# Optimization experiments

Hardware: AMD Instinct MI355X
Metric: run time of the kernel (lower is better)

The kernel has to match this reference:

```python
import jax, jax.numpy as jnp
import numpy as np
import itertools

GRID = 256          # voxel grid extent per axis (coords in [0, GRID))
KSIZE = 3           # kernel_size
OFFSETS = np.array(list(itertools.product(range(KSIZE), repeat=3)), dtype=np.int32) - (KSIZE // 2)  # [27,3]


def setup_inputs() -> dict:
    key = jax.random.key(0)
    k1, k2, k3 = jax.random.split(key, 3)
    N, Cin, Cout = 262144, 64, 64
    coords = jax.random.randint(k1, (N, 3), 0, GRID, dtype=jnp.int32)
    feats = jax.random.normal(k2, (N, Cin), dtype=jnp.float32)
    kernel = jax.random.normal(k3, (KSIZE ** 3, Cin, Cout), dtype=jnp.float32) * 0.02
    return {"coords": coords, "feats": feats, "kernel": kernel}


def reference(coords, feats, kernel):
    # Submanifold sparse conv3d: out[i] = sum_k feats[j_k(i)] @ kernel[k]
    # where coords[j_k(i)] == coords[i] + offset_k (if such a point exists).
    N = coords.shape[0]
    Cout = kernel.shape[-1]
    # Hash table: linearized voxel -> point index (-1 if empty).
    lin = (coords[:, 0] * GRID + coords[:, 1]) * GRID + coords[:, 2]
    table = jnp.full((GRID ** 3,), -1, dtype=jnp.int32).at[lin].set(
        jnp.arange(N, dtype=jnp.int32))
    out = jnp.zeros((N, Cout), dtype=feats.dtype)
    for k in range(KSIZE ** 3):
        off = jnp.asarray(OFFSETS[k])              # [3]
        nc = coords + off[None, :]                 # neighbor coords [N,3]
        in_bounds = jnp.all((nc >= 0) & (nc < GRID), axis=1)
        nlin = (nc[:, 0] * GRID + nc[:, 1]) * GRID + nc[:, 2]
        idx = table[jnp.clip(nlin, 0, GRID ** 3 - 1)]
        valid = in_bounds & (idx >= 0)
        g = feats[jnp.where(valid, idx, 0)] * valid[:, None].astype(feats.dtype)  # [N,Cin]
        out = out + g @ kernel[k]                  # [N,Cout]
    return out
```

## Files before the change

### kernel.cpp

```cpp
#include <hip/hip_runtime.h>

#define VGRID 256
#define N_TAPS 27
#define CIN 64
#define COUT 64

typedef short short8 __attribute__((ext_vector_type(8)));
typedef float float4v __attribute__((ext_vector_type(4)));

__device__ __forceinline__ short f2bf(float x) {
    unsigned u = __builtin_bit_cast(unsigned, x);
    unsigned r = (u + 0x7FFF + ((u >> 16) & 1)) >> 16;
    return (short)r;
}

__global__ void __launch_bounds__(256) build_kernel(
        const int* __restrict__ coords, int* __restrict__ table,
        unsigned* __restrict__ bits, const float* __restrict__ W,
        short* __restrict__ Wt, int n, int bt_blocks) {
    if ((int)blockIdx.x >= bt_blocks) {
        int tap = blockIdx.x - bt_blocks;
        for (int e = threadIdx.x; e < CIN * COUT; e += 256) {
            int ci = e >> 6, co = e & 63;
            int ks = ci >> 5, quad = (ci >> 3) & 3, el = ci & 7;
            Wt[((((size_t)tap * 2 + ks) * 4 + quad) * 64 + co) * 8 + el] =
                f2bf(W[((size_t)tap * CIN + ci) * COUT + co]);
        }
        return;
    }
    int i = blockIdx.x * 256 + threadIdx.x;
    if (i >= n) return;
    int lin = (coords[i * 3 + 0] * VGRID + coords[i * 3 + 1]) * VGRID + coords[i * 3 + 2];
    atomicMax(&table[lin], i);
    atomicOr(&bits[lin >> 5], 1u << (lin & 31));
}

__global__ void __launch_bounds__(256) fused_kernel(
        const int* __restrict__ coords, const int* __restrict__ table,
        const unsigned* __restrict__ bits, const float* __restrict__ feats,
        const short* __restrict__ Wt, float* __restrict__ out, int n) {
    int t = threadIdx.x;
    int lane = t & 63;
    int i = blockIdx.x * 256 + t;
    int wbase = blockIdx.x * 256 + (t & 192);

    int cx = 0, cy = 0, cz = 0;
    unsigned hitmask = 0;
    int center_idx = 0;
    if (i < n) {
        cx = coords[i * 3 + 0];
        cy = coords[i * 3 + 1];
        cz = coords[i * 3 + 2];
        int clin = (cx * VGRID + cy) * VGRID + cz;
        center_idx = table[clin];

        int zlo = cz > 0 ? cz - 1 : 0;
        int zhi = cz < VGRID - 1 ? cz + 1 : VGRID - 1;
        int wlo = zlo >> 5, whi = zhi >> 5;
        unsigned rw0[9], rw1[9];
#pragma unroll
        for (int r = 0; r < 9; ++r) {
            int nx = cx + r / 3 - 1, ny = cy + r % 3 - 1;
            bool v = ((unsigned)nx < VGRID) && ((unsigned)ny < VGRID);
            int rb = ((nx * VGRID + ny) * VGRID) >> 5;
            rw0[r] = v ? bits[rb + wlo] : 0u;
            rw1[r] = v ? bits[rb + whi] : 0u;
        }
#pragma unroll
        for (int k = 0; k < N_TAPS; ++k) {
            if (k == 13) continue;
            int nz = cz + k % 3 - 1;
            if ((unsigned)nz < VGRID) {
                unsigned wrd = ((nz >> 5) == wlo) ? rw0[k / 3] : rw1[k / 3];
                hitmask |= ((wrd >> (nz & 31)) & 1u) << k;
            }
        }
    }

    int p0 = 0, p1 = 0, p2 = 0, p3 = 0;
    {
        unsigned hm = hitmask;
        int cnt = 0;
        while (hm) {
            int k = __builtin_ctz(hm); hm &= hm - 1u;
            int nlin = ((cx + k / 9 - 1) * VGRID + (cy + (k / 3) % 3 - 1)) * VGRID
                       + (cz + k % 3 - 1);
            int j = table[nlin];
            if (cnt == 0) p0 = j; else if (cnt == 1) p1 = j;
            else if (cnt == 2) p2 = j; else if (cnt == 3) p3 = j;
            ++cnt;
        }
    }

    int packed = (cx << 16) | (cy << 8) | cz;

    unsigned gmor = hitmask;
    gmor |= (unsigned)__shfl_xor((int)gmor, 1);
    gmor |= (unsigned)__shfl_xor((int)gmor, 2);
    gmor |= (unsigned)__shfl_xor((int)gmor, 4);
    gmor |= (unsigned)__shfl_xor((int)gmor, 8);

    int m = lane & 15, quad = lane >> 4;
    const short8* Bp = (const short8*)Wt;

    for (int g = 0; g < 4; ++g) {
        int src = g * 16 + m;
        int rpk = __shfl(packed, src);
        unsigned rhm = (unsigned)__shfl((int)hitmask, src);
        int rjc = __shfl(center_idx, src);
        int rp0 = __shfl(p0, src), rp1 = __shfl(p1, src);
        int rp2 = __shfl(p2, src), rp3 = __shfl(p3, src);
        unsigned gor = (unsigned)__shfl((int)gmor, g * 16);
        gor = __builtin_amdgcn_readfirstlane(gor);

        float4v acc[4] = {{0,0,0,0},{0,0,0,0},{0,0,0,0},{0,0,0,0}};

        {
            const float* fr = feats + (size_t)rjc * CIN + quad * 8;
            float4 u0 = *(const float4*)(fr);
            float4 u1 = *(const float4*)(fr + 4);
            float4 v0 = *(const float4*)(fr + 32);
            float4 v1 = *(const float4*)(fr + 36);
            short8 a0 = {f2bf(u0.x), f2bf(u0.y), f2bf(u0.z), f2bf(u0.w),
                         f2bf(u1.x), f2bf(u1.y), f2bf(u1.z), f2bf(u1.w)};
            short8 a1 = {f2bf(v0.x), f2bf(v0.y), f2bf(v0.z), f2bf(v0.w),
                         f2bf(v1.x), f2bf(v1.y), f2bf(v1.z), f2bf(v1.w)};
#pragma unroll
            for (int nt = 0; nt < 4; ++nt) {
                short8 b0 = Bp[((13 * 2 + 0) * 4 + quad) * 64 + nt * 16 + m];
                short8 b1 = Bp[((13 * 2 + 1) * 4 + quad) * 64 + nt * 16 + m];
                acc[nt] = __builtin_amdgcn_mfma_f32_16x16x32_bf16(a0, b0, acc[nt], 0, 0, 0);
                acc[nt] = __builtin_amdgcn_mfma_f32_16x16x32_bf16(a1, b1, acc[nt], 0, 0, 0);
            }
        }

        unsigned gm = gor;
        while (gm) {
            int k = (int)__builtin_ctz(gm); gm &= gm - 1u;
            bool has = (rhm >> k) & 1u;
            short8 h0 = {0,0,0,0,0,0,0,0}, h1 = {0,0,0,0,0,0,0,0};
            if (has) {
                int rank = __builtin_popcount(rhm & ((1u << k) - 1u));
                int j2;
                if (rank == 0) j2 = rp0;
                else if (rank == 1) j2 = rp1;
                else if (rank == 2) j2 = rp2;
                else if (rank == 3) j2 = rp3;
                else {
                    int rx = (rpk >> 16) & 255, ry = (rpk >> 8) & 255, rz = rpk & 255;
                    j2 = table[((rx + k / 9 - 1) * VGRID + (ry + (k / 3) % 3 - 1)) * VGRID
                               + (rz + k % 3 - 1)];
                }
                const float* hr = feats + (size_t)j2 * CIN + quad * 8;
                float4 u0 = *(const float4*)(hr);
                float4 u1 = *(const float4*)(hr + 4);
                float4 v0 = *(const float4*)(hr + 32);
                float4 v1 = *(const float4*)(hr + 36);
                h0 = (short8){f2bf(u0.x), f2bf(u0.y), f2bf(u0.z), f2bf(u0.w),
                              f2bf(u1.x), f2bf(u1.y), f2bf(u1.z), f2bf(u1.w)};
                h1 = (short8){f2bf(v0.x), f2bf(v0.y), f2bf(v0.z), f2bf(v0.w),
                              f2bf(v1.x), f2bf(v1.y), f2bf(v1.z), f2bf(v1.w)};
            }
#pragma unroll
            for (int nt = 0; nt < 4; ++nt) {
                short8 b0 = Bp[((k * 2 + 0) * 4 + quad) * 64 + nt * 16 + m];
                short8 b1 = Bp[((k * 2 + 1) * 4 + quad) * 64 + nt * 16 + m];
                acc[nt] = __builtin_amdgcn_mfma_f32_16x16x32_bf16(h0, b0, acc[nt], 0, 0, 0);
                acc[nt] = __builtin_amdgcn_mfma_f32_16x16x32_bf16(h1, b1, acc[nt], 0, 0, 0);
            }
        }

#pragma unroll
        for (int nt = 0; nt < 4; ++nt)
#pragma unroll
            for (int r2 = 0; r2 < 4; ++r2) {
                int orow = wbase + g * 16 + quad * 4 + r2;
                if (orow < n) out[(size_t)orow * COUT + nt * 16 + m] = acc[nt][r2];
            }
    }
}

extern "C" void kernel_launch(void* const* d_in, const int* in_sizes, int n_in,
                              void* d_out, int out_size, void* d_ws, size_t ws_size,
                              hipStream_t stream) {
    const int* coords = (const int*)d_in[0];
    const float* feats = (const float*)d_in[1];
    const float* weights = (const float*)d_in[2];
    float* out = (float*)d_out;

    int n = in_sizes[0] / 3;

    char* ws = (char*)d_ws;
    size_t BITMAP_BYTES = (size_t)VGRID * VGRID * VGRID / 8;
    unsigned* bits = (unsigned*)ws;
    short* wbft = (short*)(ws + BITMAP_BYTES);
    int* table = (int*)(ws + ((size_t)4 << 20));

    hipMemsetAsync(ws, 0, BITMAP_BYTES, stream);

    int bt_blocks = (n + 255) / 256;
    build_kernel<<<bt_blocks + N_TAPS, 256, 0, stream>>>(coords, table, bits,
                                                         weights, wbft, n, bt_blocks);

    fused_kernel<<<bt_blocks, 256, 0, stream>>>(coords, table, bits, feats,
                                                wbft, out, n);
}
```

Before: 222.6 us.

## Split neighbor lookup across two threads per point and stage metadata in LDS

Each block now handles 128 points with 256 threads. Two threads cooperate per point: each loads half of the bitmap rows and does up to two table lookups, and the results are combined through shared memory. Each wave then runs two 16-row MFMA groups instead of four, which doubles the grid size and increases parallelism for the latency-bound gather phase. The cost is two block barriers, extra LDS traffic, and a launch-bounds occupancy hint that may limit registers.

```diff
diff --git a/kernel.cpp b/kernel.cpp
--- a/kernel.cpp
+++ b/kernel.cpp
@@ -4,6 +4,7 @@
 #define N_TAPS 27
 #define CIN 64
 #define COUT 64
+#define BPTS 128
 
 typedef short short8 __attribute__((ext_vector_type(8)));
 typedef float float4v __attribute__((ext_vector_type(4)));
@@ -35,82 +36,102 @@
     atomicOr(&bits[lin >> 5], 1u << (lin & 31));
 }
 
-__global__ void __launch_bounds__(256) fused_kernel(
+__global__ void __launch_bounds__(256, 8) fused_kernel(
         const int* __restrict__ coords, const int* __restrict__ table,
         const unsigned* __restrict__ bits, const float* __restrict__ feats,
         const short* __restrict__ Wt, float* __restrict__ out, int n) {
+    __shared__ int s_pk[BPTS];
+    __shared__ unsigned s_hm[2][BPTS];
+    __shared__ int s_jc[BPTS];
+    __shared__ int s_p[4][BPTS];
+
     int t = threadIdx.x;
-    int lane = t & 63;
-    int i = blockIdx.x * 256 + t;
-    int wbase = blockIdx.x * 256 + (t & 192);
+    int p = t & (BPTS - 1);
+    int h = t >> 7;
+    int i = blockIdx.x * BPTS + p;
 
     int cx = 0, cy = 0, cz = 0;
-    unsigned hitmask = 0;
-    int center_idx = 0;
+    unsigned pmask = 0;
     if (i < n) {
         cx = coords[i * 3 + 0];
         cy = coords[i * 3 + 1];
         cz = coords[i * 3 + 2];
-        int clin = (cx * VGRID + cy) * VGRID + cz;
-        center_idx = table[clin];
+        if (h == 0) s_jc[p] = table[(cx * VGRID + cy) * VGRID + cz];
 
         int zlo = cz > 0 ? cz - 1 : 0;
         int zhi = cz < VGRID - 1 ? cz + 1 : VGRID - 1;
         int wlo = zlo >> 5, whi = zhi >> 5;
-        unsigned rw0[9], rw1[9];
-#pragma unroll
-        for (int r = 0; r < 9; ++r) {
+        unsigned rwa[5], rwb[5];
+#pragma unroll
+        for (int rr = 0; rr < 5; ++rr) {
+            int r = h * 5 + rr;
             int nx = cx + r / 3 - 1, ny = cy + r % 3 - 1;
-            bool v = ((unsigned)nx < VGRID) && ((unsigned)ny < VGRID);
+            bool v = (r < 9) && ((unsigned)nx < VGRID) && ((unsigned)ny < VGRID);
             int rb = ((nx * VGRID + ny) * VGRID) >> 5;
-            rw0[r] = v ? bits[rb + wlo] : 0u;
-            rw1[r] = v ? bits[rb + whi] : 0u;
-        }
-#pragma unroll
-        for (int k = 0; k < N_TAPS; ++k) {
-            if (k == 13) continue;
-            int nz = cz + k % 3 - 1;
-            if ((unsigned)nz < VGRID) {
-                unsigned wrd = ((nz >> 5) == wlo) ? rw0[k / 3] : rw1[k / 3];
-                hitmask |= ((wrd >> (nz & 31)) & 1u) << k;
-            }
-        }
-    }
-
-    int p0 = 0, p1 = 0, p2 = 0, p3 = 0;
+            rwa[rr] = v ? bits[rb + wlo] : 0u;
+            rwb[rr] = v ? bits[rb + whi] : 0u;
+        }
+#pragma unroll
+        for (int rr = 0; rr < 5; ++rr) {
+            int r = h * 5 + rr;
+            if (r > 8) continue;
+#pragma unroll
+            for (int zz = 0; zz < 3; ++zz) {
+                int k = r * 3 + zz;
+                int nz = cz + zz - 1;
+                if (r < 9 && k != 13 && (unsigned)nz < VGRID) {
+                    unsigned wrd = ((nz >> 5) == wlo) ? rwa[rr] : rwb[rr];
+                    pmask |= ((wrd >> (nz & 31)) & 1u) << k;
+                }
+            }
+        }
+    }
+    if (h == 0) {
+        s_pk[p] = (cx << 16) | (cy << 8) | cz;
+        if (i >= n) s_jc[p] = 0;
+    }
+    s_hm[h][p] = pmask;
+    __syncthreads();
+
     {
-        unsigned hm = hitmask;
-        int cnt = 0;
-        while (hm) {
-            int k = __builtin_ctz(hm); hm &= hm - 1u;
-            int nlin = ((cx + k / 9 - 1) * VGRID + (cy + (k / 3) % 3 - 1)) * VGRID
-                       + (cz + k % 3 - 1);
-            int j = table[nlin];
-            if (cnt == 0) p0 = j; else if (cnt == 1) p1 = j;
-            else if (cnt == 2) p2 = j; else if (cnt == 3) p3 = j;
-            ++cnt;
-        }
-    }
-
-    int packed = (cx << 16) | (cy << 8) | cz;
-
-    unsigned gmor = hitmask;
-    gmor |= (unsigned)__shfl_xor((int)gmor, 1);
-    gmor |= (unsigned)__shfl_xor((int)gmor, 2);
-    gmor |= (unsigned)__shfl_xor((int)gmor, 4);
-    gmor |= (unsigned)__shfl_xor((int)gmor, 8);
-
+        unsigned hmc = s_hm[0][p] | s_hm[1][p];
+        if (h == 0) s_hm[0][p] = hmc;
+        unsigned mm = hmc;
+        if (h) { mm &= mm - 1u; if (mm) mm &= mm - 1u; }
+        int kA = -1, kB = -1;
+        if (mm) { kA = __builtin_ctz(mm); mm &= mm - 1u;
+                  if (mm) kB = __builtin_ctz(mm); }
+        int ja = 0, jb = 0;
+        if (kA >= 0)
+            ja = table[((cx + kA / 9 - 1) * VGRID + (cy + (kA / 3) % 3 - 1)) * VGRID
+                       + (cz + kA % 3 - 1)];
+        if (kB >= 0)
+            jb = table[((cx + kB / 9 - 1) * VGRID + (cy + (kB / 3) % 3 - 1)) * VGRID
+                       + (cz + kB % 3 - 1)];
+        s_p[2 * h + 0][p] = ja;
+        s_p[2 * h + 1][p] = jb;
+    }
+    __syncthreads();
+
+    int wave = t >> 6, lane = t & 63;
     int m = lane & 15, quad = lane >> 4;
     const short8* Bp = (const short8*)Wt;
-
-    for (int g = 0; g < 4; ++g) {
-        int src = g * 16 + m;
-        int rpk = __shfl(packed, src);
-        unsigned rhm = (unsigned)__shfl((int)hitmask, src);
-        int rjc = __shfl(center_idx, src);
-        int rp0 = __shfl(p0, src), rp1 = __shfl(p1, src);
-        int rp2 = __shfl(p2, src), rp3 = __shfl(p3, src);
-        unsigned gor = (unsigned)__shfl((int)gmor, g * 16);
+    int base = blockIdx.x * BPTS;
+
+    for (int gg = 0; gg < 2; ++gg) {
+        int g = wave * 2 + gg;
+        int row = g * 16 + m;
+        int rpk = s_pk[row];
+        unsigned rhm = s_hm[0][row];
+        int rjc = s_jc[row];
+        int rp0 = s_p[0][row], rp1 = s_p[1][row];
+        int rp2 = s_p[2][row], rp3 = s_p[3][row];
+
+        unsigned gor = rhm;
+        gor |= (unsigned)__shfl_xor((int)gor, 1);
+        gor |= (unsigned)__shfl_xor((int)gor, 2);
+        gor |= (unsigned)__shfl_xor((int)gor, 4);
+        gor |= (unsigned)__shfl_xor((int)gor, 8);
         gor = __builtin_amdgcn_readfirstlane(gor);
 
         float4v acc[4] = {{0,0,0,0},{0,0,0,0},{0,0,0,0},{0,0,0,0}};
@@ -174,7 +195,7 @@
         for (int nt = 0; nt < 4; ++nt)
 #pragma unroll
             for (int r2 = 0; r2 < 4; ++r2) {
-                int orow = wbase + g * 16 + quad * 4 + r2;
+                int orow = base + g * 16 + quad * 4 + r2;
                 if (orow < n) out[(size_t)orow * COUT + nt * 16 + m] = acc[nt][r2];
             }
     }
@@ -202,6 +223,7 @@
     build_kernel<<<bt_blocks + N_TAPS, 256, 0, stream>>>(coords, table, bits,
                                                          weights, wbft, n, bt_blocks);
 
-    fused_kernel<<<bt_blocks, 256, 0, stream>>>(coords, table, bits, feats,
-                                                wbft, out, n);
-}
+    int f_blocks = (n + BPTS - 1) / BPTS;
+    fused_kernel<<<f_blocks, 256, 0, stream>>>(coords, table, bits, feats,
+                                               wbft, out, n);
+}
```

New measurement: 248.8 us. +11.8%, slower.
